# Performance work log

Measured on AMD Instinct MI355X. Metric: run time of the kernel, lower is better.

## Reference

```python
import jax, jax.numpy as jnp
import numpy as np

EMBED_DIM = 12  # hardcoded in the original module


def setup_inputs() -> dict:
    key = jax.random.key(0)
    k_x, k_w, k_b, k_v = jax.random.split(key, 4)
    feature_dim = 768
    hidden_dim = 4
    feature_num = feature_dim // EMBED_DIM  # 64 fields
    batch = 32768
    x = jax.random.normal(k_x, (batch, feature_dim), dtype=jnp.float32)
    # nn.Linear(feature_dim, 1): weight [1, feature_dim], bias [1]
    W = jax.random.normal(k_w, (1, feature_dim), dtype=jnp.float32) / np.sqrt(feature_dim)
    b = jax.random.normal(k_b, (1,), dtype=jnp.float32) * 0.01
    # V: [feature_num, field_num, hidden_dim]
    V = jax.random.normal(k_v, (feature_num, feature_num, hidden_dim), dtype=jnp.float32)
    return {"x": x, "W": W, "b": b, "V": V}


def reference(x, W, b, V):
    B, D = x.shape
    F = V.shape[0]               # feature_num == field_num
    E = D // F                   # embedding_dim (12)
    # linear part: [B, 1]
    linear_part = x @ W.T + b
    # Pairwise interaction coefficients: C[i, j] = <V[i, j], V[j, i]>
    C = jnp.sum(V * jnp.swapaxes(V, 0, 1), axis=-1)          # [F, F]
    M = C * jnp.triu(jnp.ones((F, F), dtype=x.dtype), k=1)   # keep i < j only
    # sum_{i<j} (x_i . x_j) * C[i,j]  ==  sum_{j,e} Xr[b,j,e] * (sum_i Xr[b,i,e] * M[i,j])
    Xr = x.reshape(B, F, E)                                    # [B, F, E]
    T = jnp.einsum('bie,ij->bje', Xr, M)                       # [B, F, E]
    interaction = jnp.sum(Xr * T, axis=(1, 2))[:, None]        # [B, 1]
    return jax.nn.sigmoid(linear_part + interaction)
```

## Files before the change

kernel.cpp:

```cpp
#include <hip/hip_runtime.h>
#include <hip/hip_bf16.h>

#define BATCH 32768
#define NF    64
#define NE    12
#define MB    16
#define MROWS (MB*NE)
#define LSTR  68
#define NTILE (BATCH/MB)
#define GRID  512
#define TPB   (NTILE/GRID)

typedef __attribute__((ext_vector_type(8))) short short8;
typedef __attribute__((ext_vector_type(4))) float float4v;

#define WS_SHT 0
#define WS_SLT 8192
#define WS_WT  16384

__device__ __forceinline__ short bfb(float v) {
    union { __hip_bfloat16 h; short s; } u;
    u.h = __float2bfloat16(v);
    return u.s;
}

__global__ void prep_kernel(const float* __restrict__ V, const float* __restrict__ W,
                            unsigned short* __restrict__ ShT,
                            unsigned short* __restrict__ SlT,
                            float* __restrict__ WT) {
    const int idx = blockIdx.x * 256 + threadIdx.x;
    if (idx < NF * NF) {
        const int i = idx >> 6, j = idx & 63;
        const float4v a = *(const float4v*)(V + (size_t)((i << 6) | j) * 4);
        const float4v b = *(const float4v*)(V + (size_t)((j << 6) | i) * 4);
        const float s = (i == j) ? 0.0f
                      : 0.5f * (a.x * b.x + a.y * b.y + a.z * b.z + a.w * b.w);
        const __hip_bfloat16 sh = __float2bfloat16(s);
        union { __hip_bfloat16 h; unsigned short u; } uh, ul;
        uh.h = sh; ul.h = __float2bfloat16(s - __bfloat162float(sh));
        ShT[(j << 6) | i] = uh.u;
        SlT[(j << 6) | i] = ul.u;
    }
    if (idx < NF * NE) {
        const int j = idx / NE, e = idx - j * NE;
        WT[e * 64 + j] = W[idx];
    }
}

__global__ __launch_bounds__(256, 2) void ffm_mfma(
    const float* __restrict__ x,
    const float* __restrict__ bvec,
    const unsigned short* __restrict__ ShT,
    const unsigned short* __restrict__ SlT,
    const float* __restrict__ WT,
    float* __restrict__ out)
{
    __shared__ float Xs[MROWS * LSTR];
    __shared__ float red[MROWS];

    const int tid  = threadIdx.x;
    const int w    = tid >> 6;
    const int lane = tid & 63;
    const int l15  = lane & 15;
    const int q    = lane >> 4;

    short8 shf[4][2], slf[4][2];
    #pragma unroll
    for (int ns = 0; ns < 4; ++ns)
        #pragma unroll
        for (int kb = 0; kb < 2; ++kb) {
            const int off = ((ns << 4) + l15) * 64 + kb * 32 + q * 8;
            shf[ns][kb] = *(const short8*)(ShT + off);
            slf[ns][kb] = *(const short8*)(SlT + off);
        }

    float4v v[12];
    {
        const float4v* xg = (const float4v*)(x + (size_t)blockIdx.x * MB * (NF * NE));
        #pragma unroll
        for (int p = 0; p < 12; ++p) v[p] = xg[p * 256 + tid];
    }

    for (int tt = 0; tt < TPB; ++tt) {
        const int tile = tt * GRID + blockIdx.x;

        #pragma unroll
        for (int p = 0; p < 12; ++p) {
            const int fid = p * 256 + tid;
            const int b   = fid / 192;
            const int c4  = fid - b * 192;
            const int d0  = c4 * 4;
            const int i0  = d0 / 12;
            const int e0  = d0 - i0 * 12;
            float* dst = Xs + (b * NE + e0) * LSTR + i0;
            dst[0 * LSTR] = v[p].x; dst[1 * LSTR] = v[p].y;
            dst[2 * LSTR] = v[p].z; dst[3 * LSTR] = v[p].w;
        }
        __syncthreads();

        if (tt + 1 < TPB) {
            const int ntile = (tt + 1) * GRID + blockIdx.x;
            const float4v* xg = (const float4v*)(x + (size_t)ntile * MB * (NF * NE));
            #pragma unroll
            for (int p = 0; p < 12; ++p) v[p] = xg[p * 256 + tid];
        }

        #pragma unroll
        for (int ms = 0; ms < 3; ++ms) {
            const int msg  = w * 3 + ms;
            const int mrow = (msg << 4) + l15;

            short8 ah[2], al[2];
            #pragma unroll
            for (int kb = 0; kb < 2; ++kb) {
                const float4v t0 = *(const float4v*)(Xs + mrow * LSTR + kb * 32 + q * 8);
                const float4v t1 = *(const float4v*)(Xs + mrow * LSTR + kb * 32 + q * 8 + 4);
                const float a8[8] = {t0.x, t0.y, t0.z, t0.w, t1.x, t1.y, t1.z, t1.w};
                #pragma unroll
                for (int j = 0; j < 8; ++j) {
                    const float vv = a8[j];
                    const __hip_bfloat16 h = __float2bfloat16(vv);
                    ah[kb][j] = bfb(vv);
                    al[kb][j] = bfb(vv - __bfloat162float(h));
                }
            }

            float4v acc[4];
            #pragma unroll
            for (int ns = 0; ns < 4; ++ns) {
                float4v c = (float4v){0.f, 0.f, 0.f, 0.f};
                c = __builtin_amdgcn_mfma_f32_16x16x32_bf16(ah[0], shf[ns][0], c, 0, 0, 0);
                c = __builtin_amdgcn_mfma_f32_16x16x32_bf16(ah[1], shf[ns][1], c, 0, 0, 0);
                c = __builtin_amdgcn_mfma_f32_16x16x32_bf16(al[0], shf[ns][0], c, 0, 0, 0);
                c = __builtin_amdgcn_mfma_f32_16x16x32_bf16(al[1], shf[ns][1], c, 0, 0, 0);
                c = __builtin_amdgcn_mfma_f32_16x16x32_bf16(ah[0], slf[ns][0], c, 0, 0, 0);
                c = __builtin_amdgcn_mfma_f32_16x16x32_bf16(ah[1], slf[ns][1], c, 0, 0, 0);
                acc[ns] = c;
            }

            #pragma unroll
            for (int rg = 0; rg < 4; ++rg) {
                const int m = (msg << 4) + (q << 2) + rg;
                const int e = m % NE;
                float p = 0.0f;
                #pragma unroll
                for (int ns = 0; ns < 4; ++ns) {
                    const int n = (ns << 4) + l15;
                    p = fmaf(Xs[m * LSTR + n], acc[ns][rg] + WT[e * 64 + n], p);
                }
                p += __shfl_xor(p, 1);
                p += __shfl_xor(p, 2);
                p += __shfl_xor(p, 4);
                p += __shfl_xor(p, 8);
                if (l15 == 0) red[m] = p;
            }
        }
        __syncthreads();

        if (tid < MB) {
            float s = 0.0f;
            #pragma unroll
            for (int e = 0; e < NE; ++e) s += red[tid * NE + e];
            const float z = s + bvec[0];
            out[tile * MB + tid] = 1.0f / (1.0f + __expf(-z));
        }
    }
}

extern "C" void kernel_launch(void* const* d_in, const int* in_sizes, int n_in,
                              void* d_out, int out_size, void* d_ws, size_t ws_size,
                              hipStream_t stream) {
    const float* x  = (const float*)d_in[0];
    const float* W  = (const float*)d_in[1];
    const float* bb = (const float*)d_in[2];
    const float* V  = (const float*)d_in[3];
    unsigned short* ShT = (unsigned short*)((char*)d_ws + WS_SHT);
    unsigned short* SlT = (unsigned short*)((char*)d_ws + WS_SLT);
    float*          WT  = (float*)((char*)d_ws + WS_WT);
    float* out = (float*)d_out;

    prep_kernel<<<dim3(16), dim3(256), 0, stream>>>(V, W, ShT, SlT, WT);
    ffm_mfma<<<dim3(GRID), dim3(256), 0, stream>>>(x, bb, ShT, SlT, WT, out);
}
```

Before: 156.4 us.

## Double-buffer x tiles via direct global-to-LDS loads with smaller tiles

Replaces the register-staged transpose of x into LDS with direct global_load_lds DMA into a double-buffered raw-layout LDS tile. The next tile's load is issued before computing on the current one, and the output reduction for the previous tile is deferred so each iteration needs only one barrier. Tiles shrink to 8 batch rows with 192 threads and 1024 blocks, and the prep kernel permutes the S matrix so A-fragments can be gathered from the untransposed layout with stride-12 LDS reads. The aim is to overlap the global traffic with the MFMA work and to drop the register staging and transpose stores. The cost is strided, possibly bank-conflicted scalar LDS reads for the A fragments.

Measured after the change: 176.2 us. +12.6%, slower.

```diff
diff --git a/kernel.cpp b/kernel.cpp
--- a/kernel.cpp
+++ b/kernel.cpp
@@ -4,11 +4,11 @@
 #define BATCH 32768
 #define NF    64
 #define NE    12
-#define MB    16
+#define MB    8
 #define MROWS (MB*NE)
-#define LSTR  68
+#define NTHR  192
 #define NTILE (BATCH/MB)
-#define GRID  512
+#define GRID  1024
 #define TPB   (NTILE/GRID)
 
 typedef __attribute__((ext_vector_type(8))) short short8;
@@ -17,6 +17,9 @@
 #define WS_SHT 0
 #define WS_SLT 8192
 #define WS_WT  16384
+
+#define GLOBAL_AS __attribute__((address_space(1)))
+#define LDS_AS    __attribute__((address_space(3)))
 
 __device__ __forceinline__ short bfb(float v) {
     union { __hip_bfloat16 h; short s; } u;
@@ -30,16 +33,18 @@
                             float* __restrict__ WT) {
     const int idx = blockIdx.x * 256 + threadIdx.x;
     if (idx < NF * NF) {
-        const int i = idx >> 6, j = idx & 63;
-        const float4v a = *(const float4v*)(V + (size_t)((i << 6) | j) * 4);
-        const float4v b = *(const float4v*)(V + (size_t)((j << 6) | i) * 4);
-        const float s = (i == j) ? 0.0f
-                      : 0.5f * (a.x * b.x + a.y * b.y + a.z * b.z + a.w * b.w);
-        const __hip_bfloat16 sh = __float2bfloat16(s);
+        const int n  = idx >> 6, ks = idx & 63;
+        const int kb = ks >> 5,  s  = ks & 31;
+        const int i  = (kb << 5) + ((s & 7) << 2) + (s >> 3);
+        const float4v a = *(const float4v*)(V + (size_t)((i << 6) | n) * 4);
+        const float4v b = *(const float4v*)(V + (size_t)((n << 6) | i) * 4);
+        const float sv = (i == n) ? 0.0f
+                       : 0.5f * (a.x * b.x + a.y * b.y + a.z * b.z + a.w * b.w);
+        const __hip_bfloat16 sh = __float2bfloat16(sv);
         union { __hip_bfloat16 h; unsigned short u; } uh, ul;
-        uh.h = sh; ul.h = __float2bfloat16(s - __bfloat162float(sh));
-        ShT[(j << 6) | i] = uh.u;
-        SlT[(j << 6) | i] = ul.u;
+        uh.h = sh; ul.h = __float2bfloat16(sv - __bfloat162float(sh));
+        ShT[idx] = uh.u;
+        SlT[idx] = ul.u;
     }
     if (idx < NF * NE) {
         const int j = idx / NE, e = idx - j * NE;
@@ -47,7 +52,20 @@
     }
 }
 
-__global__ __launch_bounds__(256, 2) void ffm_mfma(
+__device__ __forceinline__ void dma_tile(const float* __restrict__ x, int tile,
+                                         float* dst, int w, int lane) {
+    const float4v* src = (const float4v*)(x + (size_t)tile * MB * (NF * NE));
+    #pragma unroll
+    for (int k2 = 0; k2 < 8; ++k2) {
+        const int k = w * 8 + k2;
+        const float4v* g = src + k * 64 + lane;
+        float* l = dst + k * 256 + lane * 4;
+        __builtin_amdgcn_global_load_lds((const GLOBAL_AS void*)g,
+                                         (LDS_AS void*)l, 16, 0, 0);
+    }
+}
+
+__global__ __launch_bounds__(NTHR, 3) void ffm_mfma(
     const float* __restrict__ x,
     const float* __restrict__ bvec,
     const unsigned short* __restrict__ ShT,
@@ -55,8 +73,8 @@
     const float* __restrict__ WT,
     float* __restrict__ out)
 {
-    __shared__ float Xs[MROWS * LSTR];
-    __shared__ float red[MROWS];
+    __shared__ float Xs[2][MB * NF * NE];
+    __shared__ float red[2][MROWS];
 
     const int tid  = threadIdx.x;
     const int w    = tid >> 6;
@@ -74,96 +92,85 @@
             slf[ns][kb] = *(const short8*)(SlT + off);
         }
 
-    float4v v[12];
-    {
-        const float4v* xg = (const float4v*)(x + (size_t)blockIdx.x * MB * (NF * NE));
+    dma_tile(x, blockIdx.x, Xs[0], w, lane);
+
+    for (int tt = 0; tt < TPB; ++tt) {
+        __syncthreads();
+        const int buf = tt & 1;
+
+        if (tt + 1 < TPB)
+            dma_tile(x, (tt + 1) * GRID + blockIdx.x, Xs[buf ^ 1], w, lane);
+
+        if (tt > 0 && tid < MB) {
+            float s = 0.0f;
+            #pragma unroll
+            for (int e = 0; e < NE; ++e) s += red[buf ^ 1][tid * NE + e];
+            const float z = s + bvec[0];
+            out[((tt - 1) * GRID + blockIdx.x) * MB + tid] = 1.0f / (1.0f + __expf(-z));
+        }
+
+        const float* Xb = Xs[buf];
         #pragma unroll
-        for (int p = 0; p < 12; ++p) v[p] = xg[p * 256 + tid];
+        for (int ms = 0; ms < 2; ++ms) {
+            const int msg = w * 2 + ms;
+            {
+                const int m = (msg << 4) + l15;
+                const int b = m / NE, e = m - (m / NE) * NE;
+                const float* abase = Xb + b * (NF * NE) + e + q * NE;
+
+                short8 ah[2], al[2];
+                #pragma unroll
+                for (int kb = 0; kb < 2; ++kb)
+                    #pragma unroll
+                    for (int j = 0; j < 8; ++j) {
+                        const float vv = abase[(kb * 32 + 4 * j) * NE];
+                        const __hip_bfloat16 h = __float2bfloat16(vv);
+                        ah[kb][j] = bfb(vv);
+                        al[kb][j] = bfb(vv - __bfloat162float(h));
+                    }
+
+                float4v acc[4];
+                #pragma unroll
+                for (int ns = 0; ns < 4; ++ns) {
+                    float4v c = (float4v){0.f, 0.f, 0.f, 0.f};
+                    c = __builtin_amdgcn_mfma_f32_16x16x32_bf16(ah[0], shf[ns][0], c, 0, 0, 0);
+                    c = __builtin_amdgcn_mfma_f32_16x16x32_bf16(ah[1], shf[ns][1], c, 0, 0, 0);
+                    c = __builtin_amdgcn_mfma_f32_16x16x32_bf16(al[0], shf[ns][0], c, 0, 0, 0);
+                    c = __builtin_amdgcn_mfma_f32_16x16x32_bf16(al[1], shf[ns][1], c, 0, 0, 0);
+                    c = __builtin_amdgcn_mfma_f32_16x16x32_bf16(ah[0], slf[ns][0], c, 0, 0, 0);
+                    c = __builtin_amdgcn_mfma_f32_16x16x32_bf16(ah[1], slf[ns][1], c, 0, 0, 0);
+                    acc[ns] = c;
+                }
+
+                #pragma unroll
+                for (int rg = 0; rg < 4; ++rg) {
+                    const int mm = (msg << 4) + (q << 2) + rg;
+                    const int bb2 = mm / NE, ee = mm - bb2 * NE;
+                    const float* ebase = Xb + bb2 * (NF * NE) + ee + l15 * NE;
+                    float p = 0.0f;
+                    #pragma unroll
+                    for (int ns = 0; ns < 4; ++ns) {
+                        const int n = (ns << 4) + l15;
+                        p = fmaf(ebase[(ns << 4) * NE], acc[ns][rg] + WT[ee * 64 + n], p);
+                    }
+                    p += __shfl_xor(p, 1);
+                    p += __shfl_xor(p, 2);
+                    p += __shfl_xor(p, 4);
+                    p += __shfl_xor(p, 8);
+                    if (l15 == 0) red[buf][mm] = p;
+                }
+            }
+        }
     }
 
-    for (int tt = 0; tt < TPB; ++tt) {
-        const int tile = tt * GRID + blockIdx.x;
-
+    __syncthreads();
+    if (tid < MB) {
+        const int buf = (TPB - 1) & 1;
+        float s = 0.0f;
         #pragma unroll
-        for (int p = 0; p < 12; ++p) {
-            const int fid = p * 256 + tid;
-            const int b   = fid / 192;
-            const int c4  = fid - b * 192;
-            const int d0  = c4 * 4;
-            const int i0  = d0 / 12;
-            const int e0  = d0 - i0 * 12;
-            float* dst = Xs + (b * NE + e0) * LSTR + i0;
-            dst[0 * LSTR] = v[p].x; dst[1 * LSTR] = v[p].y;
-            dst[2 * LSTR] = v[p].z; dst[3 * LSTR] = v[p].w;
-        }
-        __syncthreads();
-
-        if (tt + 1 < TPB) {
-            const int ntile = (tt + 1) * GRID + blockIdx.x;
-            const float4v* xg = (const float4v*)(x + (size_t)ntile * MB * (NF * NE));
-            #pragma unroll
-            for (int p = 0; p < 12; ++p) v[p] = xg[p * 256 + tid];
-        }
-
-        #pragma unroll
-        for (int ms = 0; ms < 3; ++ms) {
-            const int msg  = w * 3 + ms;
-            const int mrow = (msg << 4) + l15;
-
-            short8 ah[2], al[2];
-            #pragma unroll
-            for (int kb = 0; kb < 2; ++kb) {
-                const float4v t0 = *(const float4v*)(Xs + mrow * LSTR + kb * 32 + q * 8);
-                const float4v t1 = *(const float4v*)(Xs + mrow * LSTR + kb * 32 + q * 8 + 4);
-                const float a8[8] = {t0.x, t0.y, t0.z, t0.w, t1.x, t1.y, t1.z, t1.w};
-                #pragma unroll
-                for (int j = 0; j < 8; ++j) {
-                    const float vv = a8[j];
-                    const __hip_bfloat16 h = __float2bfloat16(vv);
-                    ah[kb][j] = bfb(vv);
-                    al[kb][j] = bfb(vv - __bfloat162float(h));
-                }
-            }
-
-            float4v acc[4];
-            #pragma unroll
-            for (int ns = 0; ns < 4; ++ns) {
-                float4v c = (float4v){0.f, 0.f, 0.f, 0.f};
-                c = __builtin_amdgcn_mfma_f32_16x16x32_bf16(ah[0], shf[ns][0], c, 0, 0, 0);
-                c = __builtin_amdgcn_mfma_f32_16x16x32_bf16(ah[1], shf[ns][1], c, 0, 0, 0);
-                c = __builtin_amdgcn_mfma_f32_16x16x32_bf16(al[0], shf[ns][0], c, 0, 0, 0);
-                c = __builtin_amdgcn_mfma_f32_16x16x32_bf16(al[1], shf[ns][1], c, 0, 0, 0);
-                c = __builtin_amdgcn_mfma_f32_16x16x32_bf16(ah[0], slf[ns][0], c, 0, 0, 0);
-                c = __builtin_amdgcn_mfma_f32_16x16x32_bf16(ah[1], slf[ns][1], c, 0, 0, 0);
-                acc[ns] = c;
-            }
-
-            #pragma unroll
-            for (int rg = 0; rg < 4; ++rg) {
-                const int m = (msg << 4) + (q << 2) + rg;
-                const int e = m % NE;
-                float p = 0.0f;
-                #pragma unroll
-                for (int ns = 0; ns < 4; ++ns) {
-                    const int n = (ns << 4) + l15;
-                    p = fmaf(Xs[m * LSTR + n], acc[ns][rg] + WT[e * 64 + n], p);
-                }
-                p += __shfl_xor(p, 1);
-                p += __shfl_xor(p, 2);
-                p += __shfl_xor(p, 4);
-                p += __shfl_xor(p, 8);
-                if (l15 == 0) red[m] = p;
-            }
-        }
-        __syncthreads();
-
-        if (tid < MB) {
-            float s = 0.0f;
-            #pragma unroll
-            for (int e = 0; e < NE; ++e) s += red[tid * NE + e];
-            const float z = s + bvec[0];
-            out[tile * MB + tid] = 1.0f / (1.0f + __expf(-z));
-        }
+        for (int e = 0; e < NE; ++e) s += red[buf][tid * NE + e];
+        const float z = s + bvec[0];
+        out[((TPB - 1) * GRID + blockIdx.x) * MB + tid] = 1.0f / (1.0f + __expf(-z));
     }
 }
 
@@ -180,5 +187,5 @@
     float* out = (float*)d_out;
 
     prep_kernel<<<dim3(16), dim3(256), 0, stream>>>(V, W, ShT, SlT, WT);
-    ffm_mfma<<<dim3(GRID), dim3(256), 0, stream>>>(x, bb, ShT, SlT, WT, out);
+    ffm_mfma<<<dim3(GRID), dim3(NTHR), 0, stream>>>(x, bb, ShT, SlT, WT, out);
 }
```
